# Kernel optimization log

Hardware: AMD Instinct MI355X
Metric: run time of the kernel (lower is better)

Reference implementation:

```python
import jax, jax.numpy as jnp
import numpy as np

N = 1 << 20        # number of query points
L_HIDDEN = 6       # hidden (64->64) layers, i.e. params[1:-1]
NEG_SLOPE = 0.2    # nn.LeakyReLU(0.2)

# NOTE: nn.Dropout(0.5) is treated in eval mode (identity), the standard
# convention for deterministic correctness baselines.

def _lrelu(x):
    return jnp.where(x >= 0, x, NEG_SLOPE * x)


def setup_inputs() -> dict:
    key = jax.random.key(0)
    ks = jax.random.split(key, 11)
    return {
        "points": jax.random.normal(ks[0], (N, 3), jnp.float32),
        "w0": jax.random.normal(ks[1], (3, 64), jnp.float32),
        "s0": jax.random.normal(ks[2], (64,), jnp.float32),
        "b0": jax.random.normal(ks[3], (64,), jnp.float32),
        "wh": jax.random.normal(ks[4], (L_HIDDEN, 64, 64), jnp.float32),
        "sh": jax.random.normal(ks[5], (L_HIDDEN, 64), jnp.float32),
        "bh": jax.random.normal(ks[6], (L_HIDDEN, 64), jnp.float32),
        "wo": jax.random.normal(ks[7], (64, 1), jnp.float32),
        "so": jax.random.normal(ks[8], (), jnp.float32),
        "bo": jax.random.normal(ks[9], (), jnp.float32),
    }


def reference(points, w0, s0, b0, wh, sh, bh, wo, so, bo):
    # first layer: [N,3] @ [3,64] * scale + bias -> leakyrelu
    x = _lrelu(jnp.matmul(points, w0) * s0 + b0)
    # hidden layers: small static loop over structurally distinct param sets
    for i in range(L_HIDDEN):
        x = _lrelu(jnp.matmul(x, wh[i]) * sh[i] + bh[i])
    # output layer: [N,64] @ [64,1] * scalar + scalar (no activation)
    return jnp.matmul(x, wo) * so + bo
```

## Files before the change

### kernel.cpp

```cpp
#include <hip/hip_runtime.h>


typedef _Float16 half8 __attribute__((ext_vector_type(8)));
typedef _Float16 half2v __attribute__((ext_vector_type(2)));
typedef float floatx16 __attribute__((ext_vector_type(16)));
typedef int int4v __attribute__((ext_vector_type(4)));

#define N_HID 6
#define OFF_A 0
#define OFF_B 49152
#define OFF_C 51200
#define OFF_D 52992
#define IMG_BYTES 57088
#define SETUP_TOTAL (24576 + 1024 + 448 + 2048)

__global__ __launch_bounds__(256) void setup_weights(
    const float* __restrict__ w0, const float* __restrict__ s0, const float* __restrict__ b0,
    const float* __restrict__ wh, const float* __restrict__ sh, const float* __restrict__ bh,
    const float* __restrict__ wo, const float* __restrict__ so,
    unsigned char* __restrict__ ws)
{
    int i = blockIdx.x * 256 + threadIdx.x;
    if (i < 24576) {
        int j = i & 7, lane = (i >> 3) & 63, s = (i >> 9) & 3, t = (i >> 11) & 1, l = i >> 12;
        int m = 32 * t + (lane & 31);
        int h = lane >> 5;
        int feat = 16 * s + 8 * (j >> 2) + 4 * h + (j & 3);
        ((_Float16*)(ws + OFF_A))[i] = (_Float16)(wh[(l * 64 + feat) * 64 + m] * sh[l * 64 + m]);
    } else if (i < 24576 + 1024) {
        int i2 = i - 24576;
        int j = i2 & 7, lane = (i2 >> 3) & 63, t = i2 >> 9;
        int m = 32 * t + (lane & 31);
        int k = 8 * (lane >> 5) + j;
        float v = (k < 3) ? w0[k * 64 + m] * s0[m] * 0.015625f : 0.f;
        ((_Float16*)(ws + OFF_B))[i2] = (_Float16)v;
    } else if (i < 24576 + 1024 + 448) {
        int i2 = i - 24576 - 1024;
        int r = i2 & 15, t = (i2 >> 4) & 1, h = (i2 >> 5) & 1, l = i2 >> 6;
        int feat = 32 * t + (r & 3) + 8 * ((r >> 2) & 3) + 4 * h;
        float bv = (l == 0) ? b0[feat] : bh[(l - 1) * 64 + feat];
        ((float*)(ws + OFF_C))[i2] = bv * 0.015625f;
    } else if (i < SETUP_TOTAL) {
        int i2 = i - (24576 + 1024 + 448);
        int j = i2 & 7, lane = (i2 >> 3) & 63, s = i2 >> 9;
        int h = lane >> 5;
        int feat = 16 * s + 8 * (j >> 2) + 4 * h + (j & 3);
        ((_Float16*)(ws + OFF_D))[i2] = (_Float16)(wo[feat] * so[0] * 64.f);
    }
}

static __device__ __forceinline__ int pkrtz(float a, float b) {
    auto hh = __builtin_amdgcn_cvt_pkrtz(a, b);
    int r;
    __builtin_memcpy(&r, &hh, 4);
    return r;
}

static __device__ __forceinline__ int lrelu2(int v) {
    half2v u;
    __builtin_memcpy(&u, &v, 4);
    half2v w = u * (_Float16)0.2f;
    half2v r = __builtin_elementwise_max(u, w);
    int o;
    __builtin_memcpy(&o, &r, 4);
    return o;
}

static __device__ __forceinline__ half8 as_h8(int4v v) {
    half8 r;
    __builtin_memcpy(&r, &v, 16);
    return r;
}

static __device__ __forceinline__ floatx16 mfma16(half8 a, half8 b, floatx16 c) {
    return __builtin_amdgcn_mfma_f32_32x32x16_f16(a, b, c, 0, 0, 0);
}

__global__ __launch_bounds__(512, 4) void mlp_mfma(
    const float* __restrict__ points,
    const unsigned char* __restrict__ ws,
    const float* __restrict__ bo,
    float* __restrict__ out, int n)
{
    __shared__ __align__(16) unsigned char lds[IMG_BYTES];

    {
        const uint4* src = (const uint4*)ws;
        uint4* dst = (uint4*)lds;
#pragma unroll
        for (int i = 0; i < 6; ++i) {
            int idx = threadIdx.x + 512 * i;
            dst[idx] = src[idx];
        }
        if (threadIdx.x < 496) {
            int idx = 3072 + threadIdx.x;
            dst[idx] = src[idx];
        }
    }
    __syncthreads();

    const int lane = threadIdx.x & 63;
    const int wv = threadIdx.x >> 6;
    const int p = lane & 31;
    const int h = lane >> 5;
    const int base = (blockIdx.x * 8 + wv) * 64;
    const int pt0 = base + p, pt1 = base + 32 + p;
    const int pl0 = min(pt0, n - 1), pl1 = min(pt1, n - 1);

    const half8* Wf = (const half8*)(lds + OFF_A);
    const half8* A0 = (const half8*)(lds + OFF_B);
    const floatx16* biasC = (const floatx16*)(lds + OFF_C);
    const half8* woA = (const half8*)(lds + OFF_D);

    floatx16 acc[2][2];
    int4v frv[2][4];

    {
        int4v z4 = {0, 0, 0, 0};
        int4v b0v = z4, b1v = z4;
        if (h == 0) {
            b0v[0] = pkrtz(points[3 * pl0 + 0], points[3 * pl0 + 1]);
            b0v[1] = pkrtz(points[3 * pl0 + 2], 0.f);
            b1v[0] = pkrtz(points[3 * pl1 + 0], points[3 * pl1 + 1]);
            b1v[1] = pkrtz(points[3 * pl1 + 2], 0.f);
        }
        floatx16 c0 = biasC[h * 2 + 0];
        floatx16 c1 = biasC[h * 2 + 1];
        half8 a0 = A0[lane], a1 = A0[64 + lane];
        __builtin_amdgcn_s_setprio(1);
        acc[0][0] = mfma16(a0, as_h8(b0v), c0);
        acc[0][1] = mfma16(a1, as_h8(b0v), c1);
        acc[1][0] = mfma16(a0, as_h8(b1v), c0);
        acc[1][1] = mfma16(a1, as_h8(b1v), c1);
        __builtin_amdgcn_s_setprio(0);
    }

    auto packfr = [&]() {
#pragma unroll
        for (int nt = 0; nt < 2; ++nt)
#pragma unroll
            for (int t = 0; t < 2; ++t)
#pragma unroll
                for (int rp = 0; rp < 8; ++rp) {
                    int v = pkrtz(acc[nt][t][2 * rp], acc[nt][t][2 * rp + 1]);
                    int idx = 8 * t + rp;
                    frv[nt][idx >> 2][idx & 3] = lrelu2(v);
                }
    };
    packfr();

    for (int l = 0; l < N_HID; ++l) {
        const floatx16 c0 = biasC[((l + 1) * 2 + h) * 2 + 0];
        const floatx16 c1 = biasC[((l + 1) * 2 + h) * 2 + 1];
        const half8* wl = Wf + l * 512 + lane;
        __builtin_amdgcn_s_setprio(1);
        {
            half8 w0 = wl[0], w1 = wl[256];
            half8 f0 = as_h8(frv[0][0]), f1 = as_h8(frv[1][0]);
            acc[0][0] = mfma16(w0, f0, c0);
            acc[0][1] = mfma16(w1, f0, c1);
            acc[1][0] = mfma16(w0, f1, c0);
            acc[1][1] = mfma16(w1, f1, c1);
        }
#pragma unroll
        for (int s = 1; s < 4; ++s) {
            half8 w0 = wl[s * 64], w1 = wl[256 + s * 64];
            half8 f0 = as_h8(frv[0][s]), f1 = as_h8(frv[1][s]);
            acc[0][0] = mfma16(w0, f0, acc[0][0]);
            acc[0][1] = mfma16(w1, f0, acc[0][1]);
            acc[1][0] = mfma16(w0, f1, acc[1][0]);
            acc[1][1] = mfma16(w1, f1, acc[1][1]);
        }
        __builtin_amdgcn_s_setprio(0);
        packfr();
    }

    {
        floatx16 z;
#pragma unroll
        for (int r = 0; r < 16; ++r) z[r] = 0.f;
        floatx16 o0 = z, o1 = z;
        __builtin_amdgcn_s_setprio(1);
#pragma unroll
        for (int s = 0; s < 4; ++s) {
            half8 w = woA[s * 64 + lane];
            o0 = mfma16(w, as_h8(frv[0][s]), o0);
            o1 = mfma16(w, as_h8(frv[1][s]), o1);
        }
        __builtin_amdgcn_s_setprio(0);
        const float bov = bo[0];
        if (h == 0) {
            if (pt0 < n) out[pt0] = o0[0] + bov;
            if (pt1 < n) out[pt1] = o1[0] + bov;
        }
    }
}

extern "C" void kernel_launch(void* const* d_in, const int* in_sizes, int n_in,
                              void* d_out, int out_size, void* d_ws, size_t ws_size,
                              hipStream_t stream) {
    const float* points = (const float*)d_in[0];
    const float* w0     = (const float*)d_in[1];
    const float* s0     = (const float*)d_in[2];
    const float* b0     = (const float*)d_in[3];
    const float* wh     = (const float*)d_in[4];
    const float* sh     = (const float*)d_in[5];
    const float* bh     = (const float*)d_in[6];
    const float* wo     = (const float*)d_in[7];
    const float* so     = (const float*)d_in[8];
    const float* bo     = (const float*)d_in[9];

    const int n = in_sizes[0] / 3;

    setup_weights<<<(SETUP_TOTAL + 255) / 256, 256, 0, stream>>>(
        w0, s0, b0, wh, sh, bh, wo, so, (unsigned char*)d_ws);

    const int grid = (n + 511) / 512;
    mlp_mfma<<<grid, 512, 0, stream>>>(
        points, (const unsigned char*)d_ws, bo, (float*)d_out, n);
}
```

Baseline: 128.2 us.

## Interleave two point tiles so packing overlaps MFMA and shrink output weights

The hidden-layer loop is restructured so the two 32-point tiles are offset: while one tile's MFMAs run, the other tile's fp32-to-fp16 pack and LeakyReLU run, so VALU work can overlap the matrix unit. The output weight image is reduced to a single per-half-lane copy indexed by h, which shrinks the LDS image and the staging copy. The output bias is folded into the MFMA accumulator through a broadcast LDS vector, replacing a global load. The layer loop is fully unrolled, which raises register pressure under the existing 4-waves launch bound.

```diff
diff --git a/kernel.cpp b/kernel.cpp
--- a/kernel.cpp
+++ b/kernel.cpp
@@ -11,13 +11,14 @@
 #define OFF_B 49152
 #define OFF_C 51200
 #define OFF_D 52992
-#define IMG_BYTES 57088
-#define SETUP_TOTAL (24576 + 1024 + 448 + 2048)
+#define OFF_E 53120
+#define IMG_BYTES 53184
+#define SETUP_TOTAL (24576 + 1024 + 448 + 64 + 16)
 
 __global__ __launch_bounds__(256) void setup_weights(
     const float* __restrict__ w0, const float* __restrict__ s0, const float* __restrict__ b0,
     const float* __restrict__ wh, const float* __restrict__ sh, const float* __restrict__ bh,
-    const float* __restrict__ wo, const float* __restrict__ so,
+    const float* __restrict__ wo, const float* __restrict__ so, const float* __restrict__ bo,
     unsigned char* __restrict__ ws)
 {
     int i = blockIdx.x * 256 + threadIdx.x;
@@ -40,12 +41,13 @@
         int feat = 32 * t + (r & 3) + 8 * ((r >> 2) & 3) + 4 * h;
         float bv = (l == 0) ? b0[feat] : bh[(l - 1) * 64 + feat];
         ((float*)(ws + OFF_C))[i2] = bv * 0.015625f;
+    } else if (i < 24576 + 1024 + 448 + 64) {
+        int i2 = i - (24576 + 1024 + 448);
+        int j = i2 & 7, hh = (i2 >> 3) & 1, s = i2 >> 4;
+        int feat = 16 * s + 8 * (j >> 2) + 4 * hh + (j & 3);
+        ((_Float16*)(ws + OFF_D))[i2] = (_Float16)(wo[feat] * so[0] * 64.f);
     } else if (i < SETUP_TOTAL) {
-        int i2 = i - (24576 + 1024 + 448);
-        int j = i2 & 7, lane = (i2 >> 3) & 63, s = i2 >> 9;
-        int h = lane >> 5;
-        int feat = 16 * s + 8 * (j >> 2) + 4 * h + (j & 3);
-        ((_Float16*)(ws + OFF_D))[i2] = (_Float16)(wo[feat] * so[0] * 64.f);
+        ((float*)(ws + OFF_E))[i - (24576 + 1024 + 448 + 64)] = bo[0];
     }
 }
 
@@ -76,10 +78,20 @@
     return __builtin_amdgcn_mfma_f32_32x32x16_f16(a, b, c, 0, 0, 0);
 }
 
+static __device__ __forceinline__ void packfr2(const floatx16 a[2], int4v f[4]) {
+#pragma unroll
+    for (int t = 0; t < 2; ++t)
+#pragma unroll
+        for (int rp = 0; rp < 8; ++rp) {
+            int v = pkrtz(a[t][2 * rp], a[t][2 * rp + 1]);
+            int idx = 8 * t + rp;
+            f[idx >> 2][idx & 3] = lrelu2(v);
+        }
+}
+
 __global__ __launch_bounds__(512, 4) void mlp_mfma(
     const float* __restrict__ points,
     const unsigned char* __restrict__ ws,
-    const float* __restrict__ bo,
     float* __restrict__ out, int n)
 {
     __shared__ __align__(16) unsigned char lds[IMG_BYTES];
@@ -92,7 +104,7 @@
             int idx = threadIdx.x + 512 * i;
             dst[idx] = src[idx];
         }
-        if (threadIdx.x < 496) {
+        if (threadIdx.x < 252) {
             int idx = 3072 + threadIdx.x;
             dst[idx] = src[idx];
         }
@@ -110,10 +122,11 @@
     const half8* Wf = (const half8*)(lds + OFF_A);
     const half8* A0 = (const half8*)(lds + OFF_B);
     const floatx16* biasC = (const floatx16*)(lds + OFF_C);
-    const half8* woA = (const half8*)(lds + OFF_D);
-
-    floatx16 acc[2][2];
-    int4v frv[2][4];
+    const half8* woD = (const half8*)(lds + OFF_D);
+    const floatx16* boC = (const floatx16*)(lds + OFF_E);
+
+    floatx16 acc0[2], acc1[2];
+    int4v frv0[4], frv1[4];
 
     {
         int4v z4 = {0, 0, 0, 0};
@@ -128,70 +141,67 @@
         floatx16 c1 = biasC[h * 2 + 1];
         half8 a0 = A0[lane], a1 = A0[64 + lane];
         __builtin_amdgcn_s_setprio(1);
-        acc[0][0] = mfma16(a0, as_h8(b0v), c0);
-        acc[0][1] = mfma16(a1, as_h8(b0v), c1);
-        acc[1][0] = mfma16(a0, as_h8(b1v), c0);
-        acc[1][1] = mfma16(a1, as_h8(b1v), c1);
-        __builtin_amdgcn_s_setprio(0);
-    }
-
-    auto packfr = [&]() {
-#pragma unroll
-        for (int nt = 0; nt < 2; ++nt)
-#pragma unroll
-            for (int t = 0; t < 2; ++t)
-#pragma unroll
-                for (int rp = 0; rp < 8; ++rp) {
-                    int v = pkrtz(acc[nt][t][2 * rp], acc[nt][t][2 * rp + 1]);
-                    int idx = 8 * t + rp;
-                    frv[nt][idx >> 2][idx & 3] = lrelu2(v);
-                }
-    };
-    packfr();
-
+        acc0[0] = mfma16(a0, as_h8(b0v), c0);
+        acc0[1] = mfma16(a1, as_h8(b0v), c1);
+        acc1[0] = mfma16(a0, as_h8(b1v), c0);
+        acc1[1] = mfma16(a1, as_h8(b1v), c1);
+        __builtin_amdgcn_s_setprio(0);
+    }
+
+    packfr2(acc0, frv0);
+
+#pragma unroll
     for (int l = 0; l < N_HID; ++l) {
-        const floatx16 c0 = biasC[((l + 1) * 2 + h) * 2 + 0];
-        const floatx16 c1 = biasC[((l + 1) * 2 + h) * 2 + 1];
         const half8* wl = Wf + l * 512 + lane;
-        __builtin_amdgcn_s_setprio(1);
-        {
-            half8 w0 = wl[0], w1 = wl[256];
-            half8 f0 = as_h8(frv[0][0]), f1 = as_h8(frv[1][0]);
-            acc[0][0] = mfma16(w0, f0, c0);
-            acc[0][1] = mfma16(w1, f0, c1);
-            acc[1][0] = mfma16(w0, f1, c0);
-            acc[1][1] = mfma16(w1, f1, c1);
-        }
+        floatx16 c0 = biasC[((l + 1) * 2 + h) * 2 + 0];
+        floatx16 c1 = biasC[((l + 1) * 2 + h) * 2 + 1];
+
+        __builtin_amdgcn_s_setprio(1);
+        acc0[0] = mfma16(wl[0],   as_h8(frv0[0]), c0);
+        acc0[1] = mfma16(wl[256], as_h8(frv0[0]), c1);
 #pragma unroll
         for (int s = 1; s < 4; ++s) {
-            half8 w0 = wl[s * 64], w1 = wl[256 + s * 64];
-            half8 f0 = as_h8(frv[0][s]), f1 = as_h8(frv[1][s]);
-            acc[0][0] = mfma16(w0, f0, acc[0][0]);
-            acc[0][1] = mfma16(w1, f0, acc[0][1]);
-            acc[1][0] = mfma16(w0, f1, acc[1][0]);
-            acc[1][1] = mfma16(w1, f1, acc[1][1]);
-        }
-        __builtin_amdgcn_s_setprio(0);
-        packfr();
+            acc0[0] = mfma16(wl[s * 64],       as_h8(frv0[s]), acc0[0]);
+            acc0[1] = mfma16(wl[256 + s * 64], as_h8(frv0[s]), acc0[1]);
+        }
+        __builtin_amdgcn_s_setprio(0);
+
+        packfr2(acc1, frv1);
+
+        __builtin_amdgcn_s_setprio(1);
+        acc1[0] = mfma16(wl[0],   as_h8(frv1[0]), c0);
+        acc1[1] = mfma16(wl[256], as_h8(frv1[0]), c1);
+#pragma unroll
+        for (int s = 1; s < 4; ++s) {
+            acc1[0] = mfma16(wl[s * 64],       as_h8(frv1[s]), acc1[0]);
+            acc1[1] = mfma16(wl[256 + s * 64], as_h8(frv1[s]), acc1[1]);
+        }
+        __builtin_amdgcn_s_setprio(0);
+
+        packfr2(acc0, frv0);
     }
 
     {
-        floatx16 z;
-#pragma unroll
-        for (int r = 0; r < 16; ++r) z[r] = 0.f;
-        floatx16 o0 = z, o1 = z;
-        __builtin_amdgcn_s_setprio(1);
-#pragma unroll
-        for (int s = 0; s < 4; ++s) {
-            half8 w = woA[s * 64 + lane];
-            o0 = mfma16(w, as_h8(frv[0][s]), o0);
-            o1 = mfma16(w, as_h8(frv[1][s]), o1);
-        }
-        __builtin_amdgcn_s_setprio(0);
-        const float bov = bo[0];
+        floatx16 co = boC[0];
+        __builtin_amdgcn_s_setprio(1);
+        floatx16 o0 = mfma16(woD[0 * 2 + h], as_h8(frv0[0]), co);
+#pragma unroll
+        for (int s = 1; s < 4; ++s)
+            o0 = mfma16(woD[s * 2 + h], as_h8(frv0[s]), o0);
+        __builtin_amdgcn_s_setprio(0);
+
+        packfr2(acc1, frv1);
+
+        __builtin_amdgcn_s_setprio(1);
+        floatx16 o1 = mfma16(woD[0 * 2 + h], as_h8(frv1[0]), co);
+#pragma unroll
+        for (int s = 1; s < 4; ++s)
+            o1 = mfma16(woD[s * 2 + h], as_h8(frv1[s]), o1);
+        __builtin_amdgcn_s_setprio(0);
+
         if (h == 0) {
-            if (pt0 < n) out[pt0] = o0[0] + bov;
-            if (pt1 < n) out[pt1] = o1[0] + bov;
+            if (pt0 < n) out[pt0] = o0[0];
+            if (pt1 < n) out[pt1] = o1[0];
         }
     }
 }
@@ -213,9 +223,9 @@
     const int n = in_sizes[0] / 3;
 
     setup_weights<<<(SETUP_TOTAL + 255) / 256, 256, 0, stream>>>(
-        w0, s0, b0, wh, sh, bh, wo, so, (unsigned char*)d_ws);
+        w0, s0, b0, wh, sh, bh, wo, so, bo, (unsigned char*)d_ws);
 
     const int grid = (n + 511) / 512;
     mlp_mfma<<<grid, 512, 0, stream>>>(
-        points, (const unsigned char*)d_ws, bo, (float*)d_out, n);
-}
+        points, (const unsigned char*)d_ws, (float*)d_out, n);
+}
```

After: 200.5 us. 1.56x slower.
